# Performance work log

Hardware: AMD Instinct MI355X
Metric: run time of the kernel (lower is better)

Reference implementation:

```python
import jax, jax.numpy as jnp
import numpy as np

N, S, SKV, K, V = 16, 4096, 4096, 64, 64


def setup_inputs() -> dict:
    key = jax.random.key(0)
    k1, k2, k3, k4 = jax.random.split(key, 4)
    return {
        "queries": jax.random.normal(k1, (N, S, K), dtype=jnp.float32),
        "keys": jax.random.normal(k2, (N, SKV, K), dtype=jnp.float32),
        "values": jax.random.normal(k3, (N, SKV, V), dtype=jnp.float32),
        "mask": jax.random.normal(k4, (S, SKV), dtype=jnp.float32),
    }


def reference(queries, keys, values, mask):
    # queries scaled by K^{-1/2}, then baddbmm(mask, q, k^T)
    scale = queries.shape[-1] ** -0.5
    q = queries * scale
    # scores: [N, S, SKV]; mask (S, SKV) broadcasts over batch like baddbmm
    scores = jnp.einsum('nsk,ntk->nst', q, keys) + mask
    attn_weights = jax.nn.softmax(scores, axis=-1)
    # attn: [N, S, V]; dropout_p = 0.0 (eval), needs_weights = False
    attn = jnp.einsum('nst,ntv->nsv', attn_weights, values)
    return attn
```

## Files before the change

kernel.cpp:

```cpp
#include <hip/hip_runtime.h>
#include <cstdint>
#include <cstddef>


typedef __attribute__((ext_vector_type(8))) short short8;
typedef __attribute__((ext_vector_type(4))) short short4v;
typedef __attribute__((ext_vector_type(4))) float f32x4;
typedef __attribute__((ext_vector_type(4))) unsigned int uint4v;
typedef __attribute__((ext_vector_type(2))) unsigned int uint2v;

#define DEV __device__ __forceinline__

constexpr int N_B   = 16;
constexpr int S_Q   = 4096;
constexpr int S_KV  = 4096;
constexpr int DH    = 64;
constexpr int BQ    = 128;
constexpr int BK    = 64;
constexpr int ITERS = S_KV / BK;
constexpr int KSTR  = 72;
constexpr int VSTR  = 68;

#define LOG2E 1.44269504088896340736f

DEV unsigned short f2bf(float f) {
  union { float f; unsigned int i; } x; x.f = f;
  unsigned int r = x.i + 0x7FFFu + ((x.i >> 16) & 1u);
  return (unsigned short)(r >> 16);
}

#if __has_builtin(__builtin_amdgcn_cvt_pk_bf16_f32)
typedef __attribute__((ext_vector_type(2))) __bf16 bf16x2v;
DEV unsigned int packrne(float a, float b) {
  union { bf16x2v v; unsigned int u; } x;
  x.v = __builtin_amdgcn_cvt_pk_bf16_f32(a, b);
  return x.u;
}
#else
DEV unsigned int packrne(float a, float b) {
  union { float f; unsigned int u; } ua, ub; ua.f = a; ub.f = b;
  unsigned int ra = ua.u + 0x7FFFu + ((ua.u >> 16) & 1u);
  unsigned int rb = ub.u + 0x7FFFu + ((ub.u >> 16) & 1u);
  return __builtin_amdgcn_perm(rb, ra, 0x07060302u);
}
#endif

DEV f32x4 mfma16(short4v a, short4v b, f32x4 c) {
#if __has_builtin(__builtin_amdgcn_mfma_f32_16x16x16bf16_1k)
  return __builtin_amdgcn_mfma_f32_16x16x16bf16_1k(a, b, c, 0, 0, 0);
#elif __has_builtin(__builtin_amdgcn_mfma_f32_16x16x16_bf16)
  return __builtin_amdgcn_mfma_f32_16x16x16_bf16(a, b, c, 0, 0, 0);
#else
  asm volatile("v_mfma_f32_16x16x16_bf16 %0, %1, %2, %0\n\ts_nop 7\n\ts_nop 7"
               : "+v"(c) : "v"(a), "v"(b));
  return c;
#endif
}

DEV void stageK(unsigned short* buf, const f32x4* kA, int t) {
  const int r0 = t >> 3, c = t & 7;
  uint4v d0, d1;
  d0[0] = packrne(kA[0][0], kA[0][1]); d0[1] = packrne(kA[0][2], kA[0][3]);
  d0[2] = packrne(kA[1][0], kA[1][1]); d0[3] = packrne(kA[1][2], kA[1][3]);
  d1[0] = packrne(kA[2][0], kA[2][1]); d1[1] = packrne(kA[2][2], kA[2][3]);
  d1[2] = packrne(kA[3][0], kA[3][1]); d1[3] = packrne(kA[3][2], kA[3][3]);
  *(uint4v*)&buf[r0 * KSTR + c * 8]        = d0;
  *(uint4v*)&buf[(r0 + 32) * KSTR + c * 8] = d1;
}

DEV void stageV(unsigned short* buf, const f32x4* L, int t) {
  const int a = t >> 4;
  const int x = t & 15;
  const int slot = (a + x) & 15;
#pragma unroll
  for (int j = 0; j < 4; ++j) {
    uint2v d;
    d[0] = packrne(L[0][j], L[1][j]);
    d[1] = packrne(L[2][j], L[3][j]);
    *(uint2v*)&buf[(x * 4 + j) * VSTR + slot * 4] = d;
  }
}

__global__ __launch_bounds__(256, 2)
void sdpa_fwd(const float* __restrict__ Qg,
              const float* __restrict__ Kg,
              const float* __restrict__ Vg,
              const float* __restrict__ Mg,
              float* __restrict__ Og)
{
  __shared__ __align__(16) unsigned short ldsK[2][BK * KSTR];
  __shared__ __align__(16) unsigned short ldsV[2][DH * VSTR];

  const int n    = blockIdx.y;
  const int q0   = blockIdx.x * BQ;
  const int t    = threadIdx.x;
  const int w    = t >> 6;
  const int lane = t & 63;
  const int l15  = lane & 15;
  const int quad = lane >> 4;

  short8 qfA0, qfA1, qfB0, qfB1;
  {
    const float* qp =
        Qg + ((size_t)n * S_Q + (size_t)(q0 + w * 32 + l15)) * DH + quad * 8;
#pragma unroll
    for (int j = 0; j < 8; ++j) {
      qfA0[j] = (short)f2bf(qp[j]);
      qfA1[j] = (short)f2bf(qp[32 + j]);
      qfB0[j] = (short)f2bf(qp[16 * DH + j]);
      qfB1[j] = (short)f2bf(qp[16 * DH + 32 + j]);
    }
  }

  const float* kgp = Kg + ((size_t)n * S_KV + (t >> 3)) * DH + (t & 7) * 8;
  const float* vgp =
      Vg + ((size_t)n * S_KV + (size_t)(t >> 4) * 4) * DH + (t & 15) * 4;
  const float* mrowA = Mg + (size_t)(q0 + w * 32 + l15) * S_KV + quad * 4;
  const float* mrowB = mrowA + (size_t)16 * S_KV;

  f32x4 accA[4], accB[4];
#pragma unroll
  for (int nt = 0; nt < 4; ++nt)
#pragma unroll
    for (int r = 0; r < 4; ++r) { accA[nt][r] = 0.0f; accB[nt][r] = 0.0f; }
  float lrunA = 0.0f, lrunB = 0.0f;

  f32x4 kA[4], vL[4];
  kA[0] = *(const f32x4*)(kgp);
  kA[1] = *(const f32x4*)(kgp + 4);
  kA[2] = *(const f32x4*)(kgp + 32 * DH);
  kA[3] = *(const f32x4*)(kgp + 32 * DH + 4);
#pragma unroll
  for (int i = 0; i < 4; ++i) vL[i] = *(const f32x4*)(vgp + i * DH);
  stageK(&ldsK[0][0], kA, t);
  stageV(&ldsV[0][0], vL, t);
  __syncthreads();

  for (int it = 0; it < ITERS; ++it) {
    const int p   = it & 1;
    const int kv0 = it * BK;
    const bool more = (it + 1 < ITERS);

    if (more) {
      const float* kn = kgp + (size_t)(kv0 + BK) * DH;
      kA[0] = *(const f32x4*)(kn);
      kA[1] = *(const f32x4*)(kn + 4);
      kA[2] = *(const f32x4*)(kn + 32 * DH);
      kA[3] = *(const f32x4*)(kn + 32 * DH + 4);
      const float* vn = vgp + (size_t)(kv0 + BK) * DH;
#pragma unroll
      for (int i = 0; i < 4; ++i) vL[i] = *(const f32x4*)(vn + i * DH);
    }

    f32x4 mkA[4], mkB[4];
#pragma unroll
    for (int h = 0; h < 4; ++h) {
      mkA[h] = *(const f32x4*)(mrowA + kv0 + 16 * h);
      mkB[h] = *(const f32x4*)(mrowB + kv0 + 16 * h);
    }

    short8 kf[4][2];
#pragma unroll
    for (int h = 0; h < 4; ++h)
#pragma unroll
      for (int kk = 0; kk < 2; ++kk)
        kf[h][kk] =
            *(const short8*)&ldsK[p][(l15 + 16 * h) * KSTR + (quad + 4 * kk) * 8];

    float pvA[4][4], pvB[4][4];
    float rsA = 0.0f, rsB = 0.0f;
#pragma unroll
    for (int h = 0; h < 4; ++h) {
      f32x4 cA = {0.f, 0.f, 0.f, 0.f}, cB = {0.f, 0.f, 0.f, 0.f};
      cA = __builtin_amdgcn_mfma_f32_16x16x32_bf16(kf[h][0], qfA0, cA, 0, 0, 0);
      cB = __builtin_amdgcn_mfma_f32_16x16x32_bf16(kf[h][0], qfB0, cB, 0, 0, 0);
      cA = __builtin_amdgcn_mfma_f32_16x16x32_bf16(kf[h][1], qfA1, cA, 0, 0, 0);
      cB = __builtin_amdgcn_mfma_f32_16x16x32_bf16(kf[h][1], qfB1, cB, 0, 0, 0);
#pragma unroll
      for (int r = 0; r < 4; ++r) {
        float eA = __builtin_amdgcn_exp2f(fmaf(cA[r], 0.125f, mkA[h][r]) * LOG2E);
        float eB = __builtin_amdgcn_exp2f(fmaf(cB[r], 0.125f, mkB[h][r]) * LOG2E);
        pvA[h][r] = eA; rsA += eA;
        pvB[h][r] = eB; rsB += eB;
      }
    }
    rsA += __shfl_xor(rsA, 16, 64);
    rsA += __shfl_xor(rsA, 32, 64);
    rsB += __shfl_xor(rsB, 16, 64);
    rsB += __shfl_xor(rsB, 32, 64);
    lrunA += rsA;
    lrunB += rsB;

    short4v pfA[4], pfB[4];
#pragma unroll
    for (int h = 0; h < 4; ++h) {
      union { uint2v u; short4v s; } ua, ub;
      ua.u[0] = packrne(pvA[h][0], pvA[h][1]);
      ua.u[1] = packrne(pvA[h][2], pvA[h][3]);
      ub.u[0] = packrne(pvB[h][0], pvB[h][1]);
      ub.u[1] = packrne(pvB[h][2], pvB[h][3]);
      pfA[h] = ua.s; pfB[h] = ub.s;
    }

#pragma unroll
    for (int nt = 0; nt < 4; ++nt) {
      const int vcol = l15 + 16 * nt;
      const int xr   = (l15 >> 2) + 4 * nt;
#pragma unroll
      for (int h = 0; h < 4; ++h) {
        const int slot = ((4 * h + quad) + xr) & 15;
        short4v vf = *(const short4v*)&ldsV[p][vcol * VSTR + slot * 4];
        accA[nt] = mfma16(vf, pfA[h], accA[nt]);
        accB[nt] = mfma16(vf, pfB[h], accB[nt]);
      }
    }

    if (more) {
      stageK(&ldsK[p ^ 1][0], kA, t);
      stageV(&ldsV[p ^ 1][0], vL, t);
    }
    __syncthreads();
  }

  const float invA = 1.0f / lrunA;
  const float invB = 1.0f / lrunB;
  float* obA = Og + ((size_t)n * S_Q + (size_t)(q0 + w * 32 + l15)) * DH
             + quad * 4;
  float* obB = obA + (size_t)16 * DH;
#pragma unroll
  for (int nt = 0; nt < 4; ++nt) {
    f32x4 oA, oB;
#pragma unroll
    for (int r = 0; r < 4; ++r) {
      oA[r] = accA[nt][r] * invA;
      oB[r] = accB[nt][r] * invB;
    }
    *(f32x4*)(obA + 16 * nt) = oA;
    *(f32x4*)(obB + 16 * nt) = oB;
  }
}

extern "C" void kernel_launch(void* const* d_in, const int* in_sizes, int n_in,
                              void* d_out, int out_size, void* d_ws, size_t ws_size,
                              hipStream_t stream) {
  (void)in_sizes; (void)n_in; (void)d_ws; (void)ws_size; (void)out_size;
  const float* q = (const float*)d_in[0];
  const float* k = (const float*)d_in[1];
  const float* v = (const float*)d_in[2];
  const float* m = (const float*)d_in[3];
  float* o = (float*)d_out;

  dim3 grid(S_Q / BQ, N_B);
  dim3 block(256);
  hipLaunchKernelGGL(sdpa_fwd, grid, block, 0, stream, q, k, v, m, o);
}
```

Measured before the change: 309.0 us.

## Use 512-thread blocks with one 16-row tile per wave and split K/V staging

Doubles the block to 8 waves, each owning 16 query rows instead of 32, so there are more waves per CU to hide latency. K and V staging is split between the two halves of the block. The row sum is now computed with an MFMA against a ones vector instead of shuffles, using bf16-rounded probabilities. It also adds s_setprio around the MFMA sections. In exchange, K fragments are read from LDS by twice as many waves, so reuse per wave drops, and the loop still has no running-max subtraction.

```diff
diff --git a/kernel.cpp b/kernel.cpp
--- a/kernel.cpp
+++ b/kernel.cpp
@@ -57,20 +57,20 @@
 #endif
 }
 
-DEV void stageK(unsigned short* buf, const f32x4* kA, int t) {
-  const int r0 = t >> 3, c = t & 7;
+DEV void stageK(unsigned short* buf, const f32x4* L, int tS) {
+  const int r0 = tS >> 3, c = tS & 7;
   uint4v d0, d1;
-  d0[0] = packrne(kA[0][0], kA[0][1]); d0[1] = packrne(kA[0][2], kA[0][3]);
-  d0[2] = packrne(kA[1][0], kA[1][1]); d0[3] = packrne(kA[1][2], kA[1][3]);
-  d1[0] = packrne(kA[2][0], kA[2][1]); d1[1] = packrne(kA[2][2], kA[2][3]);
-  d1[2] = packrne(kA[3][0], kA[3][1]); d1[3] = packrne(kA[3][2], kA[3][3]);
+  d0[0] = packrne(L[0][0], L[0][1]); d0[1] = packrne(L[0][2], L[0][3]);
+  d0[2] = packrne(L[1][0], L[1][1]); d0[3] = packrne(L[1][2], L[1][3]);
+  d1[0] = packrne(L[2][0], L[2][1]); d1[1] = packrne(L[2][2], L[2][3]);
+  d1[2] = packrne(L[3][0], L[3][1]); d1[3] = packrne(L[3][2], L[3][3]);
   *(uint4v*)&buf[r0 * KSTR + c * 8]        = d0;
   *(uint4v*)&buf[(r0 + 32) * KSTR + c * 8] = d1;
 }
 
-DEV void stageV(unsigned short* buf, const f32x4* L, int t) {
-  const int a = t >> 4;
-  const int x = t & 15;
+DEV void stageV(unsigned short* buf, const f32x4* L, int tS) {
+  const int a = tS >> 4;
+  const int x = tS & 15;
   const int slot = (a + x) & 15;
 #pragma unroll
   for (int j = 0; j < 4; ++j) {
@@ -81,7 +81,7 @@
   }
 }
 
-__global__ __launch_bounds__(256, 2)
+__global__ __launch_bounds__(512, 4)
 void sdpa_fwd(const float* __restrict__ Qg,
               const float* __restrict__ Kg,
               const float* __restrict__ Vg,
@@ -98,42 +98,50 @@
   const int lane = t & 63;
   const int l15  = lane & 15;
   const int quad = lane >> 4;
-
-  short8 qfA0, qfA1, qfB0, qfB1;
+  const int qrow = q0 + w * 16 + l15;
+
+  short8 qf0, qf1;
   {
-    const float* qp =
-        Qg + ((size_t)n * S_Q + (size_t)(q0 + w * 32 + l15)) * DH + quad * 8;
+    const float* qp = Qg + ((size_t)n * S_Q + (size_t)qrow) * DH + quad * 8;
 #pragma unroll
     for (int j = 0; j < 8; ++j) {
-      qfA0[j] = (short)f2bf(qp[j]);
-      qfA1[j] = (short)f2bf(qp[32 + j]);
-      qfB0[j] = (short)f2bf(qp[16 * DH + j]);
-      qfB1[j] = (short)f2bf(qp[16 * DH + 32 + j]);
-    }
-  }
-
-  const float* kgp = Kg + ((size_t)n * S_KV + (t >> 3)) * DH + (t & 7) * 8;
-  const float* vgp =
-      Vg + ((size_t)n * S_KV + (size_t)(t >> 4) * 4) * DH + (t & 15) * 4;
-  const float* mrowA = Mg + (size_t)(q0 + w * 32 + l15) * S_KV + quad * 4;
-  const float* mrowB = mrowA + (size_t)16 * S_KV;
-
-  f32x4 accA[4], accB[4];
+      qf0[j] = (short)f2bf(qp[j]);
+      qf1[j] = (short)f2bf(qp[32 + j]);
+    }
+  }
+
+  const bool isK = (w < 4);
+  const int  tS  = t & 255;
+  const float* sgp =
+      isK ? Kg + ((size_t)n * S_KV + (size_t)(tS >> 3)) * DH + (tS & 7) * 8
+          : Vg + ((size_t)n * S_KV + (size_t)(tS >> 4) * 4) * DH + (tS & 15) * 4;
+
+  const float* mrow = Mg + (size_t)qrow * S_KV + quad * 4;
+
+  f32x4 acc[4];
 #pragma unroll
   for (int nt = 0; nt < 4; ++nt)
 #pragma unroll
-    for (int r = 0; r < 4; ++r) { accA[nt][r] = 0.0f; accB[nt][r] = 0.0f; }
-  float lrunA = 0.0f, lrunB = 0.0f;
-
-  f32x4 kA[4], vL[4];
-  kA[0] = *(const f32x4*)(kgp);
-  kA[1] = *(const f32x4*)(kgp + 4);
-  kA[2] = *(const f32x4*)(kgp + 32 * DH);
-  kA[3] = *(const f32x4*)(kgp + 32 * DH + 4);
-#pragma unroll
-  for (int i = 0; i < 4; ++i) vL[i] = *(const f32x4*)(vgp + i * DH);
-  stageK(&ldsK[0][0], kA, t);
-  stageV(&ldsV[0][0], vL, t);
+    for (int r = 0; r < 4; ++r) acc[nt][r] = 0.0f;
+
+  f32x4 ls = {0.f, 0.f, 0.f, 0.f};
+  const short4v onesf = {(short)0x3F80, (short)0x3F80,
+                         (short)0x3F80, (short)0x3F80};
+
+  {
+    f32x4 L[4];
+    if (isK) {
+      L[0] = *(const f32x4*)(sgp);
+      L[1] = *(const f32x4*)(sgp + 4);
+      L[2] = *(const f32x4*)(sgp + 32 * DH);
+      L[3] = *(const f32x4*)(sgp + 32 * DH + 4);
+      stageK(&ldsK[0][0], L, tS);
+    } else {
+#pragma unroll
+      for (int i = 0; i < 4; ++i) L[i] = *(const f32x4*)(sgp + i * DH);
+      stageV(&ldsV[0][0], L, tS);
+    }
+  }
   __syncthreads();
 
   for (int it = 0; it < ITERS; ++it) {
@@ -141,66 +149,46 @@
     const int kv0 = it * BK;
     const bool more = (it + 1 < ITERS);
 
+    short4v pf[4];
+#pragma unroll
+    for (int h = 0; h < 4; ++h) {
+      const short8 kf0 =
+          *(const short8*)&ldsK[p][(l15 + 16 * h) * KSTR + quad * 8];
+      const short8 kf1 =
+          *(const short8*)&ldsK[p][(l15 + 16 * h) * KSTR + (quad + 4) * 8];
+      const f32x4 mk = *(const f32x4*)(mrow + kv0 + 16 * h);
+      f32x4 c = {0.f, 0.f, 0.f, 0.f};
+      __builtin_amdgcn_s_setprio(1);
+      c = __builtin_amdgcn_mfma_f32_16x16x32_bf16(kf0, qf0, c, 0, 0, 0);
+      c = __builtin_amdgcn_mfma_f32_16x16x32_bf16(kf1, qf1, c, 0, 0, 0);
+      __builtin_amdgcn_s_setprio(0);
+      float e[4];
+#pragma unroll
+      for (int r = 0; r < 4; ++r)
+        e[r] = __builtin_amdgcn_exp2f(fmaf(c[r], 0.125f, mk[r]) * LOG2E);
+      union { uint2v u; short4v s; } ue;
+      ue.u[0] = packrne(e[0], e[1]);
+      ue.u[1] = packrne(e[2], e[3]);
+      pf[h] = ue.s;
+    }
+
+    f32x4 L[4];
     if (more) {
-      const float* kn = kgp + (size_t)(kv0 + BK) * DH;
-      kA[0] = *(const f32x4*)(kn);
-      kA[1] = *(const f32x4*)(kn + 4);
-      kA[2] = *(const f32x4*)(kn + 32 * DH);
-      kA[3] = *(const f32x4*)(kn + 32 * DH + 4);
-      const float* vn = vgp + (size_t)(kv0 + BK) * DH;
-#pragma unroll
-      for (int i = 0; i < 4; ++i) vL[i] = *(const f32x4*)(vn + i * DH);
-    }
-
-    f32x4 mkA[4], mkB[4];
-#pragma unroll
-    for (int h = 0; h < 4; ++h) {
-      mkA[h] = *(const f32x4*)(mrowA + kv0 + 16 * h);
-      mkB[h] = *(const f32x4*)(mrowB + kv0 + 16 * h);
-    }
-
-    short8 kf[4][2];
-#pragma unroll
-    for (int h = 0; h < 4; ++h)
-#pragma unroll
-      for (int kk = 0; kk < 2; ++kk)
-        kf[h][kk] =
-            *(const short8*)&ldsK[p][(l15 + 16 * h) * KSTR + (quad + 4 * kk) * 8];
-
-    float pvA[4][4], pvB[4][4];
-    float rsA = 0.0f, rsB = 0.0f;
-#pragma unroll
-    for (int h = 0; h < 4; ++h) {
-      f32x4 cA = {0.f, 0.f, 0.f, 0.f}, cB = {0.f, 0.f, 0.f, 0.f};
-      cA = __builtin_amdgcn_mfma_f32_16x16x32_bf16(kf[h][0], qfA0, cA, 0, 0, 0);
-      cB = __builtin_amdgcn_mfma_f32_16x16x32_bf16(kf[h][0], qfB0, cB, 0, 0, 0);
-      cA = __builtin_amdgcn_mfma_f32_16x16x32_bf16(kf[h][1], qfA1, cA, 0, 0, 0);
-      cB = __builtin_amdgcn_mfma_f32_16x16x32_bf16(kf[h][1], qfB1, cB, 0, 0, 0);
-#pragma unroll
-      for (int r = 0; r < 4; ++r) {
-        float eA = __builtin_amdgcn_exp2f(fmaf(cA[r], 0.125f, mkA[h][r]) * LOG2E);
-        float eB = __builtin_amdgcn_exp2f(fmaf(cB[r], 0.125f, mkB[h][r]) * LOG2E);
-        pvA[h][r] = eA; rsA += eA;
-        pvB[h][r] = eB; rsB += eB;
+      const float* np = sgp + (size_t)(kv0 + BK) * DH;
+      if (isK) {
+        L[0] = *(const f32x4*)(np);
+        L[1] = *(const f32x4*)(np + 4);
+        L[2] = *(const f32x4*)(np + 32 * DH);
+        L[3] = *(const f32x4*)(np + 32 * DH + 4);
+      } else {
+#pragma unroll
+        for (int i = 0; i < 4; ++i) L[i] = *(const f32x4*)(np + i * DH);
       }
     }
-    rsA += __shfl_xor(rsA, 16, 64);
-    rsA += __shfl_xor(rsA, 32, 64);
-    rsB += __shfl_xor(rsB, 16, 64);
-    rsB += __shfl_xor(rsB, 32, 64);
-    lrunA += rsA;
-    lrunB += rsB;
-
-    short4v pfA[4], pfB[4];
-#pragma unroll
-    for (int h = 0; h < 4; ++h) {
-      union { uint2v u; short4v s; } ua, ub;
-      ua.u[0] = packrne(pvA[h][0], pvA[h][1]);
-      ua.u[1] = packrne(pvA[h][2], pvA[h][3]);
-      ub.u[0] = packrne(pvB[h][0], pvB[h][1]);
-      ub.u[1] = packrne(pvB[h][2], pvB[h][3]);
-      pfA[h] = ua.s; pfB[h] = ub.s;
-    }
+
+    __builtin_amdgcn_s_setprio(1);
+#pragma unroll
+    for (int h = 0; h < 4; ++h) ls = mfma16(onesf, pf[h], ls);
 
 #pragma unroll
     for (int nt = 0; nt < 4; ++nt) {
@@ -210,33 +198,26 @@
       for (int h = 0; h < 4; ++h) {
         const int slot = ((4 * h + quad) + xr) & 15;
         short4v vf = *(const short4v*)&ldsV[p][vcol * VSTR + slot * 4];
-        accA[nt] = mfma16(vf, pfA[h], accA[nt]);
-        accB[nt] = mfma16(vf, pfB[h], accB[nt]);
+        acc[nt] = mfma16(vf, pf[h], acc[nt]);
       }
     }
+    __builtin_amdgcn_s_setprio(0);
 
     if (more) {
-      stageK(&ldsK[p ^ 1][0], kA, t);
-      stageV(&ldsV[p ^ 1][0], vL, t);
+      if (isK) stageK(&ldsK[p ^ 1][0], L, tS);
+      else     stageV(&ldsV[p ^ 1][0], L, tS);
     }
     __syncthreads();
   }
 
-  const float invA = 1.0f / lrunA;
-  const float invB = 1.0f / lrunB;
-  float* obA = Og + ((size_t)n * S_Q + (size_t)(q0 + w * 32 + l15)) * DH
-             + quad * 4;
-  float* obB = obA + (size_t)16 * DH;
+  const float inv = 1.0f / ls[0];
+  float* ob = Og + ((size_t)n * S_Q + (size_t)qrow) * DH + quad * 4;
 #pragma unroll
   for (int nt = 0; nt < 4; ++nt) {
-    f32x4 oA, oB;
-#pragma unroll
-    for (int r = 0; r < 4; ++r) {
-      oA[r] = accA[nt][r] * invA;
-      oB[r] = accB[nt][r] * invB;
-    }
-    *(f32x4*)(obA + 16 * nt) = oA;
-    *(f32x4*)(obB + 16 * nt) = oB;
+    f32x4 o;
+#pragma unroll
+    for (int r = 0; r < 4; ++r) o[r] = acc[nt][r] * inv;
+    *(f32x4*)(ob + 16 * nt) = o;
   }
 }
 
@@ -251,6 +232,6 @@
   float* o = (float*)d_out;
 
   dim3 grid(S_Q / BQ, N_B);
-  dim3 block(256);
+  dim3 block(512);
   hipLaunchKernelGGL(sdpa_fwd, grid, block, 0, stream, q, k, v, m, o);
 }
```

New measurement: 287.6 us. 6.9% less time.
